# Kernel optimization log

Measured on AMD Instinct MI355X. Metric: run time of the kernel, lower is better.

Reference implementation:

```python
import jax, jax.numpy as jnp
import numpy as np

D_MODEL = 1024
N_HEADS = 16
HEAD_DIM = D_MODEL // N_HEADS  # 64
WINDOW = 128
LOCAL_BLOCK = 256
LATENT_TOKENS = 64
LATENT_D = 256
LATENT_HEADS = 4
LATENT_HD = LATENT_D // LATENT_HEADS  # 64
NEG = -1e9


def setup_inputs() -> dict:
    key = jax.random.key(0)
    ks = jax.random.split(key, 14)
    B, S = 2, 4096
    s = 0.02
    f32 = jnp.float32
    return {
        "x": jax.random.normal(ks[0], (B, S, D_MODEL), f32),
        "qkv_w": jax.random.normal(ks[1], (D_MODEL, 3 * D_MODEL), f32) * s,
        "qkv_b": jnp.zeros((3 * D_MODEL,), f32),
        "rq_w": jax.random.normal(ks[2], (D_MODEL, LATENT_D), f32) * s,
        "rq_b": jnp.zeros((LATENT_D,), f32),
        "rkv_w": jax.random.normal(ks[3], (D_MODEL, 2 * LATENT_D), f32) * s,
        "rkv_b": jnp.zeros((2 * LATENT_D,), f32),
        "rout_w": jax.random.normal(ks[4], (LATENT_D, D_MODEL), f32) * s,
        "rout_b": jnp.zeros((D_MODEL,), f32),
        "out_w": jax.random.normal(ks[5], (D_MODEL, D_MODEL), f32) * s,
        "out_b": jnp.zeros((D_MODEL,), f32),
        "gl_w": jax.random.normal(ks[6], (HEAD_DIM, 1), f32) * s,
        "gr_w": jax.random.normal(ks[7], (HEAD_DIM, 1), f32) * s,
    }


def _local_attention(q, k, v):
    # q,k,v: [B,H,S,hd]. Blockwise causal local attention: query i attends to
    # keys at distance d with 0 < d <= WINDOW (strictly past, self excluded).
    B, H, S, hd = q.shape
    bs = min(S, max(WINDOW, LOCAL_BLOCK))
    nb = S // bs  # S chosen divisible by bs
    w = WINDOW
    L = bs + w - 1  # key span per query block
    k_pad = jnp.pad(k, ((0, 0), (0, 0), (w - 1, 0), (0, 0)))
    v_pad = jnp.pad(v, ((0, 0), (0, 0), (w - 1, 0), (0, 0)))
    starts = jnp.arange(nb) * bs
    idx = starts[:, None] + jnp.arange(L)[None, :]  # [nb,L] into padded axis
    kb = k_pad[:, :, idx]  # [B,H,nb,L,hd]
    vb = v_pad[:, :, idx]
    qb = q.reshape(B, H, nb, bs, hd)
    q_pos = starts[:, None] + jnp.arange(bs)[None, :]            # [nb,bs]
    k_gpos = starts[:, None] + jnp.arange(L)[None, :] - (w - 1)   # [nb,L]
    dist = q_pos[:, :, None] - k_gpos[:, None, :]                 # [nb,bs,L]
    allowed = (dist > 0) & (dist <= w) & (k_gpos[:, None, :] >= 0)
    scale = 1.0 / np.sqrt(hd)
    scores = jnp.einsum('bhnqd,bhnkd->bhnqk', qb, kb) * scale
    scores = jnp.where(allowed, scores, NEG)
    attn = jax.nn.softmax(scores, axis=-1)
    # query 0 has no valid keys (self excluded) -> output 0 for that row
    attn = jnp.where(allowed.any(-1)[None, None, :, :, None], attn, 0.0)
    out = jnp.einsum('bhnqk,bhnkd->bhnqd', attn, vb)
    return out.reshape(B, H, S, hd)


def reference(x, qkv_w, qkv_b, rq_w, rq_b, rkv_w, rkv_b, rout_w, rout_b,
              out_w, out_b, gl_w, gr_w):
    B, S, D = x.shape
    # ---- local branch ----
    qkv = x @ qkv_w + qkv_b  # [B,S,3D]
    q, k, v = jnp.split(qkv, 3, axis=-1)
    def heads(t):
        return t.reshape(B, S, N_HEADS, HEAD_DIM).transpose(0, 2, 1, 3)
    local = _local_attention(heads(q), heads(k), heads(v))  # [B,H,S,hd]
    # ---- pooled latents ----
    chunk = -(-S // min(LATENT_TOKENS, S))  # ceil; S divisible here
    nlat = S // chunk
    pooled = x.reshape(B, nlat, chunk, D).mean(axis=2)  # [B,L,D]
    chunk_ids = jnp.arange(S) // chunk                   # [S]
    # ---- latent cross-attention ----
    rq = (x @ rq_w + rq_b).reshape(B, S, LATENT_HEADS, LATENT_HD).transpose(0, 2, 1, 3)
    rkv = pooled @ rkv_w + rkv_b
    rk, rv = jnp.split(rkv, 2, axis=-1)
    rk = rk.reshape(B, nlat, LATENT_HEADS, LATENT_HD).transpose(0, 2, 1, 3)
    rv = rv.reshape(B, nlat, LATENT_HEADS, LATENT_HD).transpose(0, 2, 1, 3)
    lscale = 1.0 / np.sqrt(LATENT_HD)
    lscores = jnp.einsum('bhsd,bhld->bhsl', rq, rk) * lscale  # [B,Hl,S,L]
    lat_allowed = jnp.arange(nlat)[None, :] < chunk_ids[:, None]  # strictly past chunks
    lscores = jnp.where(lat_allowed[None, None], lscores, NEG)
    lattn = jax.nn.softmax(lscores, axis=-1)
    lattn = jnp.where(lat_allowed.any(-1)[None, None, :, None], lattn, 0.0)
    lat_out = jnp.einsum('bhsl,bhld->bhsd', lattn, rv)  # [B,Hl,S,hdl]
    lat_out = lat_out.transpose(0, 2, 1, 3).reshape(B, S, LATENT_D)
    remote = (lat_out @ rout_w + rout_b)                 # [B,S,D]
    remote_h = remote.reshape(B, S, N_HEADS, HEAD_DIM).transpose(0, 2, 1, 3)
    # ---- learned per-head gate mixing local/remote ----
    gate = jax.nn.sigmoid(local @ gl_w + remote_h @ gr_w)  # [B,H,S,1]
    mixed = gate * local + (1.0 - gate) * remote_h
    mixed = mixed.transpose(0, 2, 1, 3).reshape(B, S, D)
    return mixed @ out_w + out_b
```

## Files before the change

### kernel.cpp

```cpp
#include <hip/hip_runtime.h>

typedef __bf16 bf16;
typedef bf16 bf16x4 __attribute__((ext_vector_type(4)));
typedef bf16 bf16x8 __attribute__((ext_vector_type(8)));
typedef float f32x4 __attribute__((ext_vector_type(4)));

#define B_ 2
#define S_ 4096
#define D_ 1024
#define QSTR 3328

__device__ __forceinline__ void gload_lds16(const void* g, void* l) {
  __builtin_amdgcn_global_load_lds((const __attribute__((address_space(1))) void*)g,
                                   (__attribute__((address_space(3))) void*)l, 16, 0, 0);
}

__device__ __forceinline__ void transpose_block(
    const float* __restrict__ in, bf16* __restrict__ out, int K, int N,
    int bx, int by, float (*tile)[33], int tx, int ty)
{
  const int nb = bx * 32, kb = by * 32;
#pragma unroll
  for (int j = 0; j < 4; j++)
    tile[ty + j * 8][tx] = in[(size_t)(kb + ty + j * 8) * N + nb + tx];
  __syncthreads();
#pragma unroll
  for (int j = 0; j < 4; j++)
    out[(size_t)(nb + ty + j * 8) * K + kb + tx] = (bf16)tile[tx][ty + j * 8];
}

__global__ __launch_bounds__(256) void prep_kernel(
    const float* __restrict__ qkv_w, const float* __restrict__ rq_w,
    const float* __restrict__ rkv_w, const float* __restrict__ rout_w,
    const float* __restrict__ out_w, const float* __restrict__ x,
    bf16* __restrict__ qkvr_wt, bf16* __restrict__ rkv_wt,
    bf16* __restrict__ rout_wt, bf16* __restrict__ out_wt,
    bf16* __restrict__ xb)
{
  __shared__ float tile[32][33];
  const int t = threadIdx.x;
  const int tx = t & 31, ty = t >> 5;
  int bid = blockIdx.x;
  if (bid < 3072) {
    transpose_block(qkv_w, qkvr_wt, 1024, 3072, bid % 96, bid / 96, tile, tx, ty);
    return;
  }
  bid -= 3072;
  if (bid < 256) {
    transpose_block(rq_w, qkvr_wt + (size_t)3072 * 1024, 1024, 256, bid % 8, bid / 8, tile, tx, ty);
    return;
  }
  bid -= 256;
  if (bid < 512) {
    transpose_block(rkv_w, rkv_wt, 1024, 512, bid % 16, bid / 16, tile, tx, ty);
    return;
  }
  bid -= 512;
  if (bid < 256) {
    transpose_block(rout_w, rout_wt, 256, 1024, bid % 32, bid / 32, tile, tx, ty);
    return;
  }
  bid -= 256;
  if (bid < 1024) {
    transpose_block(out_w, out_wt, 1024, 1024, bid % 32, bid / 32, tile, tx, ty);
    return;
  }
  bid -= 1024;
  const int n4 = B_ * S_ * 1024 / 4;
  for (int i = bid * 256 + t; i < n4; i += 2048 * 256) {
    const float4 v = ((const float4*)x)[i];
    bf16x4 o = {(bf16)v.x, (bf16)v.y, (bf16)v.z, (bf16)v.w};
    *(bf16x4*)&xb[i * 4] = o;
  }
}

template <typename OutT>
__global__ __launch_bounds__(256) void gemm_bias_kernel(
    const bf16* __restrict__ A, const bf16* __restrict__ Bt,
    const float* __restrict__ bias, OutT* __restrict__ C,
    int M, int N, int K)
{
  __shared__ __align__(16) bf16 Al[128 * 32];
  __shared__ __align__(16) bf16 Bl[128 * 32];
  const int m0 = blockIdx.x * 128;
  const int n0 = blockIdx.y * 128;
  const int t = threadIdx.x;
  const int lane = t & 63;
  const int wave = t >> 6;
  const int wr = (wave >> 1) * 64;
  const int wc = (wave & 1) * 64;
  const int r16 = lane & 15;
  const int kg = lane >> 4;

  f32x4 acc[4][4];
#pragma unroll
  for (int i = 0; i < 4; i++)
#pragma unroll
    for (int j = 0; j < 4; j++) {
      f32x4 z = {0.f, 0.f, 0.f, 0.f};
      acc[i][j] = z;
    }

  for (int k0 = 0; k0 < K; k0 += 32) {
    __syncthreads();
#pragma unroll
    for (int i = 0; i < 2; i++) {
      const int o = i * 4096 + wave * 1024 + lane * 16;
      const int r = o >> 6;
      const int cb = o & 63;
      gload_lds16((const char*)(A + (size_t)(m0 + r) * K + k0) + cb,
                  (char*)Al + i * 4096 + wave * 1024);
      gload_lds16((const char*)(Bt + (size_t)(n0 + r) * K + k0) + cb,
                  (char*)Bl + i * 4096 + wave * 1024);
    }
    __syncthreads();
    bf16x8 a[4], b[4];
#pragma unroll
    for (int i = 0; i < 4; i++)
      a[i] = *(const bf16x8*)&Al[(wr + i * 16 + r16) * 32 + kg * 8];
#pragma unroll
    for (int i = 0; i < 4; i++)
      b[i] = *(const bf16x8*)&Bl[(wc + i * 16 + r16) * 32 + kg * 8];
#pragma unroll
    for (int i = 0; i < 4; i++)
#pragma unroll
      for (int j = 0; j < 4; j++)
        acc[i][j] = __builtin_amdgcn_mfma_f32_16x16x32_bf16(a[i], b[j], acc[i][j], 0, 0, 0);
  }

  float bs[4];
#pragma unroll
  for (int j = 0; j < 4; j++) bs[j] = bias[n0 + wc + j * 16 + r16];
#pragma unroll
  for (int i = 0; i < 4; i++)
#pragma unroll
    for (int j = 0; j < 4; j++)
#pragma unroll
      for (int r = 0; r < 4; r++) {
        const int row = m0 + wr + i * 16 + kg * 4 + r;
        const int col = n0 + wc + j * 16 + r16;
        C[(size_t)row * N + col] = (OutT)(acc[i][j][r] + bs[j]);
      }
}

template <typename OutT>
__global__ __launch_bounds__(512, 1) void gemm8_kernel(
    const bf16* __restrict__ A, const bf16* __restrict__ Bt,
    const float* __restrict__ bias, OutT* __restrict__ C,
    int M, int N, int K)
{
  __shared__ __align__(16) bf16 Al[2][256 * 64];
  __shared__ __align__(16) bf16 Bl[2][256 * 64];

  const int nbx = gridDim.x;
  const int nwg = nbx * gridDim.y;
  int bid = blockIdx.y * nbx + blockIdx.x;
  bid = (bid & 7) * (nwg >> 3) + (bid >> 3);
  const int m0 = (bid % nbx) * 256;
  const int n0 = (bid / nbx) * 256;

  const int t = threadIdx.x;
  const int lane = t & 63;
  const int w = t >> 6;
  const int wm = w >> 2;
  const int wn = w & 3;
  const int l15 = lane & 15;
  const int kg = lane >> 4;

  const int srow = t >> 3;
  const int schunk = (t & 7) ^ (srow & 7);
  const bf16* Aaddr = A + (size_t)(m0 + srow) * K + schunk * 8;
  const bf16* Baddr = Bt + (size_t)(n0 + srow) * K + schunk * 8;

  const int NT = K >> 6;
  const int NITER = NT >> 1;

  const int arow = wm * 128 + l15;
  const int brow = wn * 64 + l15;
  const int c0 = (kg ^ (l15 & 7)) * 16;
  const int c1 = ((4 + kg) ^ (l15 & 7)) * 16;

  f32x4 acc[8][4];
#pragma unroll
  for (int i = 0; i < 8; i++)
#pragma unroll
    for (int j = 0; j < 4; j++) { f32x4 z = {0, 0, 0, 0}; acc[i][j] = z; }

#define STG_A(buf, q, kt) gload_lds16(Aaddr + (size_t)(q) * 64 * K + (kt) * 64, \
                                      (char*)&Al[buf][0] + (q) * 8192 + w * 1024)
#define STG_B(buf, q, kt) gload_lds16(Baddr + (size_t)(q) * 64 * K + (kt) * 64, \
                                      (char*)&Bl[buf][0] + (q) * 8192 + w * 1024)
#define RD_A(buf, aq) \
  _Pragma("unroll") for (int ii = 0; ii < 4; ii++) { \
    const char* p_ = (const char*)&Al[buf][0] + (size_t)(arow + (aq) * 64 + ii * 16) * 128; \
    af[ii][0] = *(const bf16x8*)(p_ + c0); \
    af[ii][1] = *(const bf16x8*)(p_ + c1); }
#define RD_B(buf) \
  _Pragma("unroll") for (int jj = 0; jj < 4; jj++) { \
    const char* p_ = (const char*)&Bl[buf][0] + (size_t)(brow + jj * 16) * 128; \
    bfr[jj][0] = *(const bf16x8*)(p_ + c0); \
    bfr[jj][1] = *(const bf16x8*)(p_ + c1); }
#define MM(iofs, j0) \
  _Pragma("unroll") for (int ii = 0; ii < 4; ii++) \
  _Pragma("unroll") for (int jj = (j0); jj < (j0) + 2; jj++) { \
    acc[(iofs) + ii][jj] = __builtin_amdgcn_mfma_f32_16x16x32_bf16(af[ii][0], bfr[jj][0], acc[(iofs) + ii][jj], 0, 0, 0); \
    acc[(iofs) + ii][jj] = __builtin_amdgcn_mfma_f32_16x16x32_bf16(af[ii][1], bfr[jj][1], acc[(iofs) + ii][jj], 0, 0, 0); }
#define BARX __builtin_amdgcn_s_barrier()
#define LGKM0 do { asm volatile("s_waitcnt lgkmcnt(0)" ::: "memory"); \
                   __builtin_amdgcn_sched_barrier(0); } while (0)
#define PRI1 __builtin_amdgcn_s_setprio(1)
#define PRI0 __builtin_amdgcn_s_setprio(0)

#pragma unroll
  for (int q = 0; q < 4; q++) { STG_B(0, q, 0); }
#pragma unroll
  for (int q = 0; q < 4; q++) { STG_A(0, q, 0); }
#pragma unroll
  for (int q = 0; q < 4; q++) { STG_B(1, q, 1); }
#pragma unroll
  for (int q = 0; q < 4; q++) { STG_A(1, q, 1); }
  asm volatile("s_waitcnt vmcnt(8)" ::: "memory");
  BARX;

  bf16x8 af[4][2], bfr[4][2];

  for (int it = 0; it < NITER; it++) {
    const int kt0 = 2 * it;
    const bool st = (it + 1) < NITER;

    RD_A(0, 0); RD_B(0);
    BARX; LGKM0; PRI1; MM(0, 0); PRI0; BARX;
    if (st) { STG_B(0, 0, kt0 + 2); STG_B(0, 1, kt0 + 2); }
    PRI1; MM(0, 2); PRI0; BARX;
    RD_A(0, 1);
    if (st) { STG_B(0, 2, kt0 + 2); STG_B(0, 3, kt0 + 2); }
    BARX; LGKM0; PRI1; MM(4, 0); PRI0; BARX;
    if (st) { STG_A(0, 0, kt0 + 2); STG_A(0, 2, kt0 + 2); }
    PRI1; MM(4, 2); PRI0;
    asm volatile("s_waitcnt vmcnt(6)" ::: "memory");
    BARX;

    RD_A(1, 0); RD_B(1);
    if (st) { STG_A(0, 1, kt0 + 2); STG_A(0, 3, kt0 + 2); }
    BARX; LGKM0; PRI1; MM(0, 0); PRI0; BARX;
    if (st) { STG_B(1, 0, kt0 + 3); STG_B(1, 1, kt0 + 3); }
    PRI1; MM(0, 2); PRI0; BARX;
    RD_A(1, 1);
    if (st) { STG_B(1, 2, kt0 + 3); STG_B(1, 3, kt0 + 3); }
    BARX; LGKM0; PRI1; MM(4, 0); PRI0; BARX;
    if (st) { STG_A(1, 0, kt0 + 3); STG_A(1, 1, kt0 + 3);
              STG_A(1, 2, kt0 + 3); STG_A(1, 3, kt0 + 3); }
    PRI1; MM(4, 2); PRI0;
    asm volatile("s_waitcnt vmcnt(8)" ::: "memory");
    BARX;
  }

#undef STG_A
#undef STG_B
#undef RD_A
#undef RD_B
#undef MM
#undef BARX
#undef LGKM0
#undef PRI1
#undef PRI0

  float bs[4];
#pragma unroll
  for (int j = 0; j < 4; j++) bs[j] = bias[n0 + wn * 64 + j * 16 + l15];
#pragma unroll
  for (int i = 0; i < 8; i++)
#pragma unroll
    for (int j = 0; j < 4; j++)
#pragma unroll
      for (int rr = 0; rr < 4; rr++) {
        const int row = m0 + wm * 128 + i * 16 + kg * 4 + rr;
        const int col = n0 + wn * 64 + j * 16 + l15;
        C[(size_t)row * N + col] = (OutT)(acc[i][j][rr] + bs[j]);
      }
}

__global__ __launch_bounds__(256) void pool_rkv_kernel(
    const bf16* __restrict__ xb, const bf16* __restrict__ rkv_wt,
    const float* __restrict__ rkv_b, bf16* __restrict__ rkvb)
{
  __shared__ float prow[1024];
  const int blk = blockIdx.x;
  const int b = blk >> 6, lt = blk & 63;
  const int t = threadIdx.x;

  const bf16* px = xb + ((size_t)b * S_ + lt * 64) * 1024 + t * 4;
  float s0 = 0.f, s1 = 0.f, s2 = 0.f, s3 = 0.f;
#pragma unroll
  for (int c = 0; c < 64; c++) {
    bf16x4 v = *(const bf16x4*)(px + (size_t)c * 1024);
    s0 += (float)v[0]; s1 += (float)v[1]; s2 += (float)v[2]; s3 += (float)v[3];
  }
  prow[t * 4 + 0] = s0 * 0.015625f;
  prow[t * 4 + 1] = s1 * 0.015625f;
  prow[t * 4 + 2] = s2 * 0.015625f;
  prow[t * 4 + 3] = s3 * 0.015625f;
  __syncthreads();

  const int n = blockIdx.y * 256 + t;
  const bf16* wcol = rkv_wt + (size_t)n * 1024;
  float s = rkv_b[n];
#pragma unroll 4
  for (int k = 0; k < 1024; k += 8) {
    bf16x8 wv = *(const bf16x8*)(wcol + k);
#pragma unroll
    for (int j = 0; j < 8; j++) s += prow[k + j] * (float)wv[j];
  }
  rkvb[(size_t)blk * 512 + n] = (bf16)s;
}

__global__ __launch_bounds__(256) void latent_attn_kernel(
    const bf16* __restrict__ qkvrb, const bf16* __restrict__ rkvb,
    bf16* __restrict__ latout)
{
  __shared__ float rq_s[256];
  __shared__ float attn_s[4][64];
  const int blk = blockIdx.x;
  const int b = blk >> 12, s = blk & 4095;
  const int t = threadIdx.x;
  const int h = t >> 6, l = t & 63;
  const int cid = s >> 6;
  rq_s[t] = (float)qkvrb[((size_t)b * S_ + s) * QSTR + 3072 + t];
  __syncthreads();
  float val = -1e30f;
  if (l < cid) {
    const bf16* kr = rkvb + (size_t)(b * 64 + l) * 512 + h * 64;
    float sum = 0.f;
#pragma unroll
    for (int c = 0; c < 8; c++) {
      bf16x8 kv = *(const bf16x8*)(kr + c * 8);
#pragma unroll
      for (int j = 0; j < 8; j++) sum += rq_s[h * 64 + c * 8 + j] * (float)kv[j];
    }
    val = sum * 0.125f;
  }
  float mx = val;
#pragma unroll
  for (int off = 32; off; off >>= 1) mx = fmaxf(mx, __shfl_xor(mx, off));
  const float p = (l < cid) ? __expf(val - mx) : 0.f;
  float sm = p;
#pragma unroll
  for (int off = 32; off; off >>= 1) sm += __shfl_xor(sm, off);
  attn_s[h][l] = (sm > 0.f) ? p / sm : 0.f;
  __syncthreads();
  float o = 0.f;
  const bf16* vb = rkvb + (size_t)b * 64 * 512 + 256 + h * 64 + l;
  for (int lat = 0; lat < cid; lat++) o += attn_s[h][lat] * (float)vb[(size_t)lat * 512];
  latout[((size_t)b * S_ + s) * 256 + h * 64 + l] = (bf16)o;
}

__global__ __launch_bounds__(256) void local_attn_mfma(
    const bf16* __restrict__ qkv, bf16* __restrict__ localb)
{
  __shared__ __align__(16) bf16 Kl[128 * 72];
  __shared__ __align__(16) bf16 Vt[64 * 136];

  const int q0 = blockIdx.x * 128;
  const int h  = blockIdx.y;
  const int b  = blockIdx.z;
  const int t  = threadIdx.x;
  const int w  = t >> 6;
  const int l  = t & 63;
  const int g  = l >> 4;
  const int l15 = l & 15;

  const bf16* qbase = qkv + (size_t)b * S_ * QSTR + h * 64;
  const bf16* kbase = qbase + 1024;
  const bf16* vbase = qbase + 2048;

  bf16* PlW = &Kl[w * 32 * 72];

  const int kq = (t & 31) * 4;
  const int dh = (t >> 5) * 8;

  bf16x8 qf[2][2];
#pragma unroll
  for (int qg = 0; qg < 2; qg++)
#pragma unroll
    for (int db = 0; db < 2; db++)
      qf[qg][db] = *(const bf16x8*)(qbase + (size_t)(q0 + w * 32 + qg * 16 + l15) * QSTR + db * 32 + g * 8);

  float m_[2][4], l_[2][4];
  f32x4 accO[2][4];
#pragma unroll
  for (int qg = 0; qg < 2; qg++) {
#pragma unroll
    for (int r = 0; r < 4; r++) { m_[qg][r] = -1e30f; l_[qg][r] = 0.f; }
#pragma unroll
    for (int dt = 0; dt < 4; dt++) { f32x4 z = {0,0,0,0}; accO[qg][dt] = z; }
  }

  const int tstart = (q0 == 0) ? 1 : 0;

  bf16x8 kreg[4], vreg[4];
  {
    const int base = q0 - 128 + tstart * 128;
#pragma unroll
    for (int i = 0; i < 4; i++) {
      const int c = i * 256 + t;
      const int kk = c >> 3, dc = c & 7;
      kreg[i] = *(const bf16x8*)(kbase + (size_t)(base + kk) * QSTR + dc * 8);
    }
#pragma unroll
    for (int i = 0; i < 4; i++)
      vreg[i] = *(const bf16x8*)(vbase + (size_t)(base + kq + i) * QSTR + dh);
  }

  for (int tile = tstart; tile < 2; tile++) {
    __syncthreads();
#pragma unroll
    for (int i = 0; i < 4; i++) {
      const int c = i * 256 + t;
      const int kk = c >> 3, dc = c & 7;
      *(bf16x8*)&Kl[kk * 72 + dc * 8] = kreg[i];
    }
#pragma unroll
    for (int j = 0; j < 8; j++) {
      bf16x4 wv = {vreg[0][j], vreg[1][j], vreg[2][j], vreg[3][j]};
      *(bf16x4*)&Vt[(dh + j) * 136 + kq] = wv;
    }
    __syncthreads();
    if (tile == 0) {
#pragma unroll
      for (int i = 0; i < 4; i++) {
        const int c = i * 256 + t;
        const int kk = c >> 3, dc = c & 7;
        kreg[i] = *(const bf16x8*)(kbase + (size_t)(q0 + kk) * QSTR + dc * 8);
      }
#pragma unroll
      for (int i = 0; i < 4; i++)
        vreg[i] = *(const bf16x8*)(vbase + (size_t)(q0 + kq + i) * QSTR + dh);
    }

    const int kt_lo = (tile == 0) ? 2 * w : 0;
    const int kt_hi = (tile == 0) ? 8 : 2 * w + 2;
    const int nkt = kt_hi - kt_lo;

    f32x4 s[2][8];
#pragma unroll
    for (int qg = 0; qg < 2; qg++)
#pragma unroll
      for (int kk = 0; kk < 8; kk++) { f32x4 z = {0,0,0,0}; s[qg][kk] = z; }

#pragma unroll
    for (int kk = 0; kk < 8; kk++) {
      if (kk >= nkt) continue;
      const int kt = kt_lo + kk;
      const bf16x8 kf0 = *(const bf16x8*)&Kl[(kt * 16 + l15) * 72 + g * 8];
      const bf16x8 kf1 = *(const bf16x8*)&Kl[(kt * 16 + l15) * 72 + 32 + g * 8];
      s[0][kk] = __builtin_amdgcn_mfma_f32_16x16x32_bf16(qf[0][0], kf0, s[0][kk], 0, 0, 0);
      s[0][kk] = __builtin_amdgcn_mfma_f32_16x16x32_bf16(qf[0][1], kf1, s[0][kk], 0, 0, 0);
      s[1][kk] = __builtin_amdgcn_mfma_f32_16x16x32_bf16(qf[1][0], kf0, s[1][kk], 0, 0, 0);
      s[1][kk] = __builtin_amdgcn_mfma_f32_16x16x32_bf16(qf[1][1], kf1, s[1][kk], 0, 0, 0);
    }
    asm volatile("s_waitcnt lgkmcnt(0)" ::: "memory");
    __builtin_amdgcn_s_barrier();

#pragma unroll
    for (int qg = 0; qg < 2; qg++) {
#pragma unroll
      for (int kk = 0; kk < 8; kk++) {
        if (kk >= nkt) continue;
        const int kr = (kt_lo + kk) * 16 + l15;
#pragma unroll
        for (int r = 0; r < 4; r++) {
          const int qr = w * 32 + qg * 16 + g * 4 + r;
          const bool ok = (tile == 0) ? (kr >= qr) : (kr < qr);
          s[qg][kk][r] = ok ? s[qg][kk][r] * 0.125f : -1e9f;
        }
      }
      float corr[4];
#pragma unroll
      for (int r = 0; r < 4; r++) {
        float v = -1e30f;
#pragma unroll
        for (int kk = 0; kk < 8; kk++) { if (kk >= nkt) continue; v = fmaxf(v, s[qg][kk][r]); }
        v = fmaxf(v, __shfl_xor(v, 1));
        v = fmaxf(v, __shfl_xor(v, 2));
        v = fmaxf(v, __shfl_xor(v, 4));
        v = fmaxf(v, __shfl_xor(v, 8));
        const float mn = fmaxf(m_[qg][r], v);
        corr[r] = __expf(m_[qg][r] - mn);
        m_[qg][r] = mn;
      }
      float rs[4] = {0.f, 0.f, 0.f, 0.f};
#pragma unroll
      for (int kk = 0; kk < 8; kk++) {
        if (kk >= nkt) continue;
        const int kt = kt_lo + kk;
#pragma unroll
        for (int r = 0; r < 4; r++) {
          const float sv = s[qg][kk][r];
          const float p = (sv > -5e8f) ? __expf(sv - m_[qg][r]) : 0.f;
          rs[r] += p;
          PlW[(g * 4 + r) * 136 + kt * 16 + l15] = (bf16)p;
        }
      }
#pragma unroll
      for (int r = 0; r < 4; r++) {
        float v = rs[r];
        v += __shfl_xor(v, 1); v += __shfl_xor(v, 2);
        v += __shfl_xor(v, 4); v += __shfl_xor(v, 8);
        l_[qg][r] = l_[qg][r] * corr[r] + v;
#pragma unroll
        for (int dt = 0; dt < 4; dt++) accO[qg][dt][r] *= corr[r];
      }
      asm volatile("s_waitcnt lgkmcnt(0)" ::: "memory");
      __builtin_amdgcn_sched_barrier(0);
      const int kc_lo = (tile == 0) ? w : 0;
      const int kc_hi = (tile == 0) ? 4 : w + 1;
#pragma unroll
      for (int kc = 0; kc < 4; kc++) {
        if (kc < kc_lo || kc >= kc_hi) continue;
        const bf16x8 pa = *(const bf16x8*)&PlW[l15 * 136 + kc * 32 + g * 8];
#pragma unroll
        for (int dt = 0; dt < 4; dt++) {
          const bf16x8 vf = *(const bf16x8*)&Vt[(dt * 16 + l15) * 136 + kc * 32 + g * 8];
          accO[qg][dt] = __builtin_amdgcn_mfma_f32_16x16x32_bf16(pa, vf, accO[qg][dt], 0, 0, 0);
        }
      }
    }
  }

  bf16* outp = localb + ((size_t)b * S_ + q0 + w * 32) * 1024 + h * 64;
#pragma unroll
  for (int qg = 0; qg < 2; qg++)
#pragma unroll
    for (int r = 0; r < 4; r++) {
      const float inv = (l_[qg][r] > 0.f) ? 1.f / l_[qg][r] : 0.f;
#pragma unroll
      for (int dt = 0; dt < 4; dt++)
        outp[(size_t)(qg * 16 + g * 4 + r) * 1024 + dt * 16 + l15] = (bf16)(accO[qg][dt][r] * inv);
    }
}

__global__ __launch_bounds__(1024) void gate_mix_kernel(
    const bf16* __restrict__ localb, const bf16* __restrict__ remote,
    const float* __restrict__ glw, const float* __restrict__ grw,
    bf16* __restrict__ mixed)
{
  const int blk = blockIdx.x;
  const int b = blk >> 12, s = blk & 4095;
  const int t = threadIdx.x;
  const int d = t & 63;
  const size_t idx = ((size_t)b * S_ + s) * 1024 + t;
  const float lf = (float)localb[idx], rf = (float)remote[idx];
  float part = lf * glw[d] + rf * grw[d];
#pragma unroll
  for (int off = 32; off; off >>= 1) part += __shfl_xor(part, off);
  const float g = 1.f / (1.f + __expf(-part));
  mixed[idx] = (bf16)(g * lf + (1.f - g) * rf);
}

extern "C" void kernel_launch(void* const* d_in, const int* in_sizes, int n_in,
                              void* d_out, int out_size, void* d_ws, size_t ws_size,
                              hipStream_t stream)
{
  const float* x      = (const float*)d_in[0];
  const float* qkv_w  = (const float*)d_in[1];
  const float* qkv_b  = (const float*)d_in[2];
  const float* rq_w   = (const float*)d_in[3];
  const float* rq_b   = (const float*)d_in[4];
  const float* rkv_w  = (const float*)d_in[5];
  const float* rkv_b  = (const float*)d_in[6];
  const float* rout_w = (const float*)d_in[7];
  const float* rout_b = (const float*)d_in[8];
  const float* out_w  = (const float*)d_in[9];
  const float* out_b  = (const float*)d_in[10];
  const float* gl_w   = (const float*)d_in[11];
  const float* gr_w   = (const float*)d_in[12];

  char* w = (char*)d_ws;
  bf16* qkvr_wt = (bf16*)w; w += (size_t)QSTR * 1024 * 2;
  bf16* rkv_wt  = (bf16*)w; w += (size_t)512 * 1024 * 2;
  bf16* rout_wt = (bf16*)w; w += (size_t)1024 * 256 * 2;
  bf16* out_wt  = (bf16*)w; w += (size_t)1024 * 1024 * 2;
  float* qkvr_b = (float*)w; w += (size_t)QSTR * 4;
  bf16* xb      = (bf16*)w; w += (size_t)B_ * S_ * 1024 * 2;
  bf16* qkvrb   = (bf16*)w; w += (size_t)B_ * S_ * QSTR * 2;
  bf16* rkvb    = (bf16*)w; w += (size_t)B_ * 64 * 512 * 2;
  bf16* latout  = (bf16*)w; w += (size_t)B_ * S_ * 256 * 2;
  bf16* remote  = (bf16*)w; w += (size_t)B_ * S_ * 1024 * 2;
  bf16* localb  = (bf16*)w; w += (size_t)B_ * S_ * 1024 * 2;
  bf16* mixed   = qkvrb;

  hipMemcpyAsync(qkvr_b, qkv_b, 3072 * sizeof(float), hipMemcpyDeviceToDevice, stream);
  hipMemcpyAsync(qkvr_b + 3072, rq_b, 256 * sizeof(float), hipMemcpyDeviceToDevice, stream);

  prep_kernel<<<dim3(7168), 256, 0, stream>>>(qkv_w, rq_w, rkv_w, rout_w, out_w, x,
                                              qkvr_wt, rkv_wt, rout_wt, out_wt, xb);

  gemm8_kernel<bf16><<<dim3(32, 13), 512, 0, stream>>>(xb, qkvr_wt, qkvr_b, qkvrb, B_ * S_, QSTR, 1024);
  pool_rkv_kernel<<<dim3(128, 2), 256, 0, stream>>>(xb, rkv_wt, rkv_b, rkvb);
  latent_attn_kernel<<<dim3(B_ * S_), 256, 0, stream>>>(qkvrb, rkvb, latout);
  gemm_bias_kernel<bf16><<<dim3(64, 8), 256, 0, stream>>>(latout, rout_wt, rout_b, remote, B_ * S_, 1024, 256);
  local_attn_mfma<<<dim3(S_ / 128, 16, B_), 256, 0, stream>>>(qkvrb, localb);
  gate_mix_kernel<<<dim3(B_ * S_), 1024, 0, stream>>>(localb, remote, gl_w, gr_w, mixed);
  gemm_bias_kernel<float><<<dim3(64, 8), 256, 0, stream>>>(mixed, out_wt, out_b, (float*)d_out, B_ * S_, 1024, 1024);
}
```

Baseline: 267.6 us.

## Fuse gate mixing into local attention and fold pooling/bias copies into prep

The gate-mix kernel is removed. Local attention now reads the remote projection and applies the per-head sigmoid gate in its epilogue, which saves a full write and read of the local output buffer plus one launch. Pooling and the rkv projection move into extra prep_kernel blocks that read fp32 x and the untransposed rkv_w directly, so the rkv weight transpose and the separate pool kernel are dropped. The bias memcpys are replaced by a prep block. In exchange, the epilogue does more work and more loads inside the attention kernel, and the fp32 pooling blocks read more bytes than the old bf16 path.

Measured after the change: 347.1 us. 29.7% more time.

```diff
diff --git a/kernel.cpp b/kernel.cpp
--- a/kernel.cpp
+++ b/kernel.cpp
@@ -33,11 +33,14 @@
     const float* __restrict__ qkv_w, const float* __restrict__ rq_w,
     const float* __restrict__ rkv_w, const float* __restrict__ rout_w,
     const float* __restrict__ out_w, const float* __restrict__ x,
-    bf16* __restrict__ qkvr_wt, bf16* __restrict__ rkv_wt,
-    bf16* __restrict__ rout_wt, bf16* __restrict__ out_wt,
-    bf16* __restrict__ xb)
+    const float* __restrict__ qkv_b, const float* __restrict__ rq_b,
+    const float* __restrict__ rkv_b,
+    bf16* __restrict__ qkvr_wt, bf16* __restrict__ rout_wt,
+    bf16* __restrict__ out_wt, bf16* __restrict__ xb,
+    float* __restrict__ qkvr_b, bf16* __restrict__ rkvb)
 {
-  __shared__ float tile[32][33];
+  __shared__ float smem[1056];
+  float (*tile)[33] = (float(*)[33])smem;
   const int t = threadIdx.x;
   const int tx = t & 31, ty = t >> 5;
   int bid = blockIdx.x;
@@ -51,11 +54,6 @@
     return;
   }
   bid -= 256;
-  if (bid < 512) {
-    transpose_block(rkv_w, rkv_wt, 1024, 512, bid % 16, bid / 16, tile, tx, ty);
-    return;
-  }
-  bid -= 512;
   if (bid < 256) {
     transpose_block(rout_w, rout_wt, 256, 1024, bid % 32, bid / 32, tile, tx, ty);
     return;
@@ -66,11 +64,46 @@
     return;
   }
   bid -= 1024;
-  const int n4 = B_ * S_ * 1024 / 4;
-  for (int i = bid * 256 + t; i < n4; i += 2048 * 256) {
-    const float4 v = ((const float4*)x)[i];
-    bf16x4 o = {(bf16)v.x, (bf16)v.y, (bf16)v.z, (bf16)v.w};
-    *(bf16x4*)&xb[i * 4] = o;
+  if (bid < 2048) {
+    const int n4 = B_ * S_ * 1024 / 4;
+    for (int i = bid * 256 + t; i < n4; i += 2048 * 256) {
+      const float4 v = ((const float4*)x)[i];
+      bf16x4 o = {(bf16)v.x, (bf16)v.y, (bf16)v.z, (bf16)v.w};
+      *(bf16x4*)&xb[i * 4] = o;
+    }
+    return;
+  }
+  bid -= 2048;
+  if (bid < 128) {
+    float* prow = smem;
+    const int b = bid >> 6, lt = bid & 63;
+    const float* px = x + ((size_t)b * S_ + lt * 64) * 1024 + t * 4;
+    float4 s4 = {0.f, 0.f, 0.f, 0.f};
+#pragma unroll
+    for (int c = 0; c < 64; c++) {
+      const float4 v = *(const float4*)(px + (size_t)c * 1024);
+      s4.x += v.x; s4.y += v.y; s4.z += v.z; s4.w += v.w;
+    }
+    prow[t * 4 + 0] = s4.x * 0.015625f;
+    prow[t * 4 + 1] = s4.y * 0.015625f;
+    prow[t * 4 + 2] = s4.z * 0.015625f;
+    prow[t * 4 + 3] = s4.w * 0.015625f;
+    __syncthreads();
+    float s0 = rkv_b[2 * t], s1 = rkv_b[2 * t + 1];
+#pragma unroll 4
+    for (int k = 0; k < 1024; k++) {
+      const float2 wv = *(const float2*)&rkv_w[(size_t)k * 512 + 2 * t];
+      const float p = prow[k];
+      s0 += p * wv.x; s1 += p * wv.y;
+    }
+    rkvb[(size_t)bid * 512 + 2 * t] = (bf16)s0;
+    rkvb[(size_t)bid * 512 + 2 * t + 1] = (bf16)s1;
+    return;
+  }
+  bid -= 128;
+  {
+    for (int i = t; i < 3072; i += 256) qkvr_b[i] = qkv_b[i];
+    if (t < 256) qkvr_b[3072 + t] = rq_b[t];
   }
 }
 
@@ -280,40 +313,6 @@
       }
 }
 
-__global__ __launch_bounds__(256) void pool_rkv_kernel(
-    const bf16* __restrict__ xb, const bf16* __restrict__ rkv_wt,
-    const float* __restrict__ rkv_b, bf16* __restrict__ rkvb)
-{
-  __shared__ float prow[1024];
-  const int blk = blockIdx.x;
-  const int b = blk >> 6, lt = blk & 63;
-  const int t = threadIdx.x;
-
-  const bf16* px = xb + ((size_t)b * S_ + lt * 64) * 1024 + t * 4;
-  float s0 = 0.f, s1 = 0.f, s2 = 0.f, s3 = 0.f;
-#pragma unroll
-  for (int c = 0; c < 64; c++) {
-    bf16x4 v = *(const bf16x4*)(px + (size_t)c * 1024);
-    s0 += (float)v[0]; s1 += (float)v[1]; s2 += (float)v[2]; s3 += (float)v[3];
-  }
-  prow[t * 4 + 0] = s0 * 0.015625f;
-  prow[t * 4 + 1] = s1 * 0.015625f;
-  prow[t * 4 + 2] = s2 * 0.015625f;
-  prow[t * 4 + 3] = s3 * 0.015625f;
-  __syncthreads();
-
-  const int n = blockIdx.y * 256 + t;
-  const bf16* wcol = rkv_wt + (size_t)n * 1024;
-  float s = rkv_b[n];
-#pragma unroll 4
-  for (int k = 0; k < 1024; k += 8) {
-    bf16x8 wv = *(const bf16x8*)(wcol + k);
-#pragma unroll
-    for (int j = 0; j < 8; j++) s += prow[k + j] * (float)wv[j];
-  }
-  rkvb[(size_t)blk * 512 + n] = (bf16)s;
-}
-
 __global__ __launch_bounds__(256) void latent_attn_kernel(
     const bf16* __restrict__ qkvrb, const bf16* __restrict__ rkvb,
     bf16* __restrict__ latout)
@@ -354,8 +353,10 @@
   latout[((size_t)b * S_ + s) * 256 + h * 64 + l] = (bf16)o;
 }
 
-__global__ __launch_bounds__(256) void local_attn_mfma(
-    const bf16* __restrict__ qkv, bf16* __restrict__ localb)
+__global__ __launch_bounds__(256) void local_attn_gate(
+    const bf16* __restrict__ qkv, const bf16* __restrict__ remote,
+    const float* __restrict__ glw, const float* __restrict__ grw,
+    bf16* __restrict__ mixedb)
 {
   __shared__ __align__(16) bf16 Kl[128 * 72];
   __shared__ __align__(16) bf16 Vt[64 * 136];
@@ -527,34 +528,37 @@
     }
   }
 
-  bf16* outp = localb + ((size_t)b * S_ + q0 + w * 32) * 1024 + h * 64;
+  float glv[4], grv[4];
+#pragma unroll
+  for (int dt = 0; dt < 4; dt++) {
+    glv[dt] = glw[dt * 16 + l15];
+    grv[dt] = grw[dt * 16 + l15];
+  }
+  bf16* outp = mixedb + ((size_t)b * S_ + q0 + w * 32) * 1024 + h * 64;
+  const bf16* rbase = remote + ((size_t)b * S_ + q0 + w * 32) * 1024 + h * 64;
 #pragma unroll
   for (int qg = 0; qg < 2; qg++)
 #pragma unroll
     for (int r = 0; r < 4; r++) {
+      const int row = qg * 16 + g * 4 + r;
       const float inv = (l_[qg][r] > 0.f) ? 1.f / l_[qg][r] : 0.f;
+      float lv[4], rv[4];
+      float part = 0.f;
+#pragma unroll
+      for (int dt = 0; dt < 4; dt++) {
+        lv[dt] = accO[qg][dt][r] * inv;
+        rv[dt] = (float)rbase[(size_t)row * 1024 + dt * 16 + l15];
+        part += lv[dt] * glv[dt] + rv[dt] * grv[dt];
+      }
+      part += __shfl_xor(part, 1);
+      part += __shfl_xor(part, 2);
+      part += __shfl_xor(part, 4);
+      part += __shfl_xor(part, 8);
+      const float gg = 1.f / (1.f + __expf(-part));
 #pragma unroll
       for (int dt = 0; dt < 4; dt++)
-        outp[(size_t)(qg * 16 + g * 4 + r) * 1024 + dt * 16 + l15] = (bf16)(accO[qg][dt][r] * inv);
-    }
-}
-
-__global__ __launch_bounds__(1024) void gate_mix_kernel(
-    const bf16* __restrict__ localb, const bf16* __restrict__ remote,
-    const float* __restrict__ glw, const float* __restrict__ grw,
-    bf16* __restrict__ mixed)
-{
-  const int blk = blockIdx.x;
-  const int b = blk >> 12, s = blk & 4095;
-  const int t = threadIdx.x;
-  const int d = t & 63;
-  const size_t idx = ((size_t)b * S_ + s) * 1024 + t;
-  const float lf = (float)localb[idx], rf = (float)remote[idx];
-  float part = lf * glw[d] + rf * grw[d];
-#pragma unroll
-  for (int off = 32; off; off >>= 1) part += __shfl_xor(part, off);
-  const float g = 1.f / (1.f + __expf(-part));
-  mixed[idx] = (bf16)(g * lf + (1.f - g) * rf);
+        outp[(size_t)row * 1024 + dt * 16 + l15] = (bf16)(gg * lv[dt] + (1.f - gg) * rv[dt]);
+    }
 }
 
 extern "C" void kernel_launch(void* const* d_in, const int* in_sizes, int n_in,
@@ -577,7 +581,6 @@
 
   char* w = (char*)d_ws;
   bf16* qkvr_wt = (bf16*)w; w += (size_t)QSTR * 1024 * 2;
-  bf16* rkv_wt  = (bf16*)w; w += (size_t)512 * 1024 * 2;
   bf16* rout_wt = (bf16*)w; w += (size_t)1024 * 256 * 2;
   bf16* out_wt  = (bf16*)w; w += (size_t)1024 * 1024 * 2;
   float* qkvr_b = (float*)w; w += (size_t)QSTR * 4;
@@ -586,20 +589,15 @@
   bf16* rkvb    = (bf16*)w; w += (size_t)B_ * 64 * 512 * 2;
   bf16* latout  = (bf16*)w; w += (size_t)B_ * S_ * 256 * 2;
   bf16* remote  = (bf16*)w; w += (size_t)B_ * S_ * 1024 * 2;
-  bf16* localb  = (bf16*)w; w += (size_t)B_ * S_ * 1024 * 2;
-  bf16* mixed   = qkvrb;
-
-  hipMemcpyAsync(qkvr_b, qkv_b, 3072 * sizeof(float), hipMemcpyDeviceToDevice, stream);
-  hipMemcpyAsync(qkvr_b + 3072, rq_b, 256 * sizeof(float), hipMemcpyDeviceToDevice, stream);
-
-  prep_kernel<<<dim3(7168), 256, 0, stream>>>(qkv_w, rq_w, rkv_w, rout_w, out_w, x,
-                                              qkvr_wt, rkv_wt, rout_wt, out_wt, xb);
+  bf16* mixedb  = (bf16*)w; w += (size_t)B_ * S_ * 1024 * 2;
+
+  prep_kernel<<<dim3(6785), 256, 0, stream>>>(qkv_w, rq_w, rkv_w, rout_w, out_w, x,
+                                              qkv_b, rq_b, rkv_b,
+                                              qkvr_wt, rout_wt, out_wt, xb, qkvr_b, rkvb);
 
   gemm8_kernel<bf16><<<dim3(32, 13), 512, 0, stream>>>(xb, qkvr_wt, qkvr_b, qkvrb, B_ * S_, QSTR, 1024);
-  pool_rkv_kernel<<<dim3(128, 2), 256, 0, stream>>>(xb, rkv_wt, rkv_b, rkvb);
   latent_attn_kernel<<<dim3(B_ * S_), 256, 0, stream>>>(qkvrb, rkvb, latout);
   gemm_bias_kernel<bf16><<<dim3(64, 8), 256, 0, stream>>>(latout, rout_wt, rout_b, remote, B_ * S_, 1024, 256);
-  local_attn_mfma<<<dim3(S_ / 128, 16, B_), 256, 0, stream>>>(qkvrb, localb);
-  gate_mix_kernel<<<dim3(B_ * S_), 1024, 0, stream>>>(localb, remote, gl_w, gr_w, mixed);
-  gemm_bias_kernel<float><<<dim3(64, 8), 256, 0, stream>>>(mixed, out_wt, out_b, (float*)d_out, B_ * S_, 1024, 1024);
-}
+  local_attn_gate<<<dim3(S_ / 128, 16, B_), 256, 0, stream>>>(qkvrb, remote, gl_w, gr_w, mixedb);
+  gemm_bias_kernel<float><<<dim3(64, 8), 256, 0, stream>>>(mixedb, out_wt, out_b, (float*)d_out, B_ * S_, 1024, 1024);
+}
```
